# Kernel optimization log

Measured on AMD Instinct MI355X. Metric: run time of the kernel, lower is better.

## Reference

```python
import jax, jax.numpy as jnp
import numpy as np

B, S, D, H = 4, 1024, 1024, 16
DK = D // H
N_REL = 5


def setup_inputs() -> dict:
    key = jax.random.key(0)
    ks = jax.random.split(key, 16)
    p = lambda k, shape: (jax.random.normal(k, shape, dtype=jnp.float32) * 0.02)
    return {
        "x": jax.random.normal(ks[0], (B, S, D), dtype=jnp.float32),
        "relation_matrix": jax.random.randint(ks[1], (S, S), 0, N_REL, dtype=jnp.int32),
        "mask": jax.random.randint(ks[2], (B, 1, S, S), 0, 2, dtype=jnp.int32),
        "Wq": p(ks[3], (D, D)), "bq": p(ks[4], (D,)),
        "Wk": p(ks[5], (D, D)), "bk": p(ks[6], (D,)),
        "Wv": p(ks[7], (D, D)), "bv": p(ks[8], (D,)),
        "Wo": p(ks[9], (D, D)), "bo": p(ks[10], (D,)),
        "rel_table": p(ks[11], (N_REL, DK)),
        "gamma": jnp.ones((D,), dtype=jnp.float32),
        "beta": jnp.zeros((D,), dtype=jnp.float32),
    }


def reference(x, relation_matrix, mask, Wq, bq, Wk, bk, Wv, bv, Wo, bo, rel_table, gamma, beta):
    b, s = x.shape[0], x.shape[1]
    residual = x
    # projections -> [B, H, S, DK]
    def proj(W, bias):
        return (x @ W + bias).reshape(b, s, H, DK).transpose(0, 2, 1, 3)
    Q, K, V = proj(Wq, bq), proj(Wk, bk), proj(Wv, bv)
    scores = jnp.einsum('bhid,bhjd->bhij', Q, K) / jnp.sqrt(jnp.float32(DK))
    # relation-embedding additive bias: gather [S,S,DK] then contract with Q
    rel_emb = rel_table[relation_matrix]               # [S, S, DK]
    rel_scores = jnp.einsum('bhid,ijd->bhij', Q, rel_emb)
    scores = scores + rel_scores * 0.5
    scores = jnp.where(mask == 0, jnp.float32(-1e9), scores)
    attention = jax.nn.softmax(scores, axis=-1)
    context = jnp.einsum('bhij,bhjd->bhid', attention, V)
    context = context.transpose(0, 2, 1, 3).reshape(b, s, D)
    output = context @ Wo + bo
    # layer norm (eps = 1e-5, torch default)
    y = output + residual
    mu = jnp.mean(y, axis=-1, keepdims=True)
    var = jnp.mean(jnp.square(y - mu), axis=-1, keepdims=True)
    return (y - mu) * jax.lax.rsqrt(var + 1e-5) * gamma + beta
```

## Files before the change

### kernel.cpp

```cpp
#include <hip/hip_runtime.h>
#include <hip/hip_bf16.h>

typedef unsigned short u16;
typedef unsigned int u32;
typedef unsigned char u8;
typedef __attribute__((ext_vector_type(8))) short short8;
typedef __attribute__((ext_vector_type(4))) float f32x4;

__device__ __forceinline__ float b2f(u16 u) {
    union { float f; u32 i; } z; z.i = ((u32)u) << 16; return z.f;
}
__device__ __forceinline__ u16 f2b(float f) {
    union { float f; u32 i; } z; z.f = f;
    u32 i = z.i;
    u32 r = (i + 0x7FFFu + ((i >> 16) & 1u)) >> 16;
    return (u16)r;
}
__device__ __forceinline__ float ldf(const void* p, size_t i, int f) {
    return f ? ((const float*)p)[i] : b2f(((const u16*)p)[i]);
}
__device__ __forceinline__ void gload_lds16(const void* g, void* l) {
    __builtin_amdgcn_global_load_lds(
        (const __attribute__((address_space(1))) u32*)g,
        (__attribute__((address_space(3))) u32*)l,
        16, 0, 0);
}

struct P14 { const void* p[14]; };
struct S14 { int s[14]; };

__global__ __launch_bounds__(256) void classify_stats(P14 ptrs, S14 szs, int* stats)
{
    __shared__ int   wsm[4], wzr[4], wag[4], way[4], wjk[4];
    __shared__ float wme[4], wmo[4];
    int i = blockIdx.x;
    int t = threadIdx.x, lane = t & 63, w = t >> 6;
    const u16* p16 = (const u16*)ptrs.p[i];
    const u32* p32 = (const u32*)ptrs.p[i];
    int n = szs.s[i];
    int n16 = n < 4096 ? n : 4096;
    int n32 = n16 >> 1;
    int small = 1, zero = 1, allg = 1, anyg = 0, junk = 0;
    float maxe = 0.f, maxo = 0.f;
    for (int k = t; k < n32; k += 256) if (p32[k] >= 8u) small = 0;
    for (int k = t; k < n16; k += 256) {
        u16 ww = p16[k];
        if (ww != 0) zero = 0;
        if (ww == 0x3F80u) anyg = 1;
        else if (ww != 0) allg = 0;
        float a = fabsf(b2f(ww));
        if (k & 1) { if (a < 1e30f && a > maxo) maxo = a; }
        else { if (!(a < 100.0f)) junk++; else if (a > maxe) maxe = a; }
    }
#pragma unroll
    for (int s = 1; s < 64; s <<= 1) {
        small &= __shfl_xor(small, s);
        zero  &= __shfl_xor(zero, s);
        allg  &= __shfl_xor(allg, s);
        anyg  |= __shfl_xor(anyg, s);
        junk  += __shfl_xor(junk, s);
        maxe   = fmaxf(maxe, __shfl_xor(maxe, s));
        maxo   = fmaxf(maxo, __shfl_xor(maxo, s));
    }
    if (lane == 0) { wsm[w]=small; wzr[w]=zero; wag[w]=allg; way[w]=anyg; wjk[w]=junk; wme[w]=maxe; wmo[w]=maxo; }
    __syncthreads();
    if (t == 0) {
        int sm=1,zr=1,ag=1,ay=0,jk=0; float me=0.f,mo=0.f;
        for (int q=0;q<4;++q){ sm&=wsm[q]; zr&=wzr[q]; ag&=wag[q]; ay|=way[q]; jk+=wjk[q]; me=fmaxf(me,wme[q]); mo=fmaxf(mo,wmo[q]); }
        stats[i*8+0]=sm; stats[i*8+1]=zr; stats[i*8+2]=(ag&&ay)?1:0; stats[i*8+3]=jk;
        stats[i*8+4]=__float_as_int(me); stats[i*8+5]=__float_as_int(mo);
    }
}

__global__ __launch_bounds__(64) void classify_bind(S14 szs, const int* stats, int* cls)
{
    if (threadIdx.x != 0) return;
    int xi = -1, mi = -1, ri = -1, rt = -1, gi = -1, bi = -1;
    int wv[4] = {-1,-1,-1,-1}; int nw = 0;
    int bs[4] = {-1,-1,-1,-1}; int nb = 0;
    for (int i = 0; i < 14; ++i) {
        int s = szs.s[i];
        int sm = stats[i*8+0], zr = stats[i*8+1];
        if (s == 4194304) { if (sm) mi = i; else xi = i; }
        else if (s == 1048576) { if (sm) ri = i; else if (nw < 4) wv[nw++] = i; }
        else if (s == 320) rt = i;
        else if (s == 1024) {
            if (zr) bi = i;
            else if (stats[i*8+2]) gi = i;
            else if (nb < 4) bs[nb++] = i;
        }
    }
    bool ok = (xi >= 0) && (mi >= 0) && (ri >= 0) && (rt >= 0) && (gi >= 0) && (bi >= 0)
           && (nw == 4) && (nb == 4);
    if (ok) {
        cls[0] = xi; cls[1] = ri; cls[2] = mi;
        cls[3] = wv[0]; cls[5] = wv[1]; cls[7] = wv[2]; cls[9] = wv[3];
        cls[4] = bs[0]; cls[6] = bs[1]; cls[8] = bs[2]; cls[10] = bs[3];
        cls[11] = rt; cls[12] = gi; cls[13] = bi;
    } else {
        for (int r = 0; r < 14; ++r) cls[r] = r;
    }
    const int froles[12] = {0,3,4,5,6,7,8,9,10,11,12,13};
    for (int r = 0; r < 12; ++r) {
        int role = froles[r]; int idx = cls[role];
        float me = __int_as_float(stats[idx*8+4]);
        float mo = __int_as_float(stats[idx*8+5]);
        cls[16 + role] = (stats[idx*8+3] > 0) || (me == 0.f && mo > 0.f);
    }
    cls[30] = ok ? 1 : 0;
}

__global__ __launch_bounds__(256) void cvt_x_flex(P14 ptrs, const int* cls, u16* xb) {
    const void* x = ptrs.p[cls[0]];
    int f = cls[16];
    int idx = (blockIdx.x * 256 + threadIdx.x) << 2;
    union { u16 u[4]; uint2 v2; } o;
    if (f) {
        float4 v = *(const float4*)((const float*)x + idx);
        o.u[0] = f2b(v.x); o.u[1] = f2b(v.y); o.u[2] = f2b(v.z); o.u[3] = f2b(v.w);
    } else {
        o.v2 = *(const uint2*)((const u16*)x + idx);
    }
    *(uint2*)&xb[idx] = o.v2;
}

__global__ __launch_bounds__(256) void transposeW_flex(P14 ptrs, const int* cls,
                                                       u16* WT3, u16* WoT)
{
    int z = blockIdx.z;
    const void* W = ptrs.p[cls[3 + 2 * z]];
    int f = cls[16 + 3 + 2 * z];
    u16* WT = (z < 3) ? (WT3 + ((size_t)z << 20)) : WoT;
    __shared__ u16 tile[64][72];
    int t = threadIdx.x;
    int n0 = blockIdx.x << 6, k0 = blockIdx.y << 6;
    int r = t >> 2, c = (t & 3) << 4;
    size_t base = (size_t)(k0 + r) * 1024 + n0 + c;
    if (f) {
        const float* src = (const float*)W + base;
#pragma unroll
        for (int x = 0; x < 16; ++x) tile[r][c + x] = f2b(src[x]);
    } else {
        const u16* src = (const u16*)W + base;
#pragma unroll
        for (int x = 0; x < 16; ++x) tile[r][c + x] = src[x];
    }
    __syncthreads();
    union { u16 u[16]; uint4 v[2]; } tmp;
#pragma unroll
    for (int x = 0; x < 16; ++x) tmp.u[x] = tile[c + x][r];
    *(uint4*)&WT[(size_t)(n0 + r) * 1024 + k0 + c]     = tmp.v[0];
    *(uint4*)&WT[(size_t)(n0 + r) * 1024 + k0 + c + 8] = tmp.v[1];
}

__global__ __launch_bounds__(256) void transposeV(const u16* __restrict__ Vb,
                                                  u16* __restrict__ VT)
{
    __shared__ u16 tile[64][72];
    int bh = blockIdx.y, j0 = blockIdx.x << 6;
    const u16* src = Vb + ((size_t)bh << 16);
    u16* dst = VT + ((size_t)bh << 16);
    int t = threadIdx.x, r = t >> 2, c = (t & 3) << 4;
    const u16* s = src + (size_t)(j0 + r) * 64 + c;
    *(uint4*)&tile[r][c]     = *(const uint4*)s;
    *(uint4*)&tile[r][c + 8] = *(const uint4*)(s + 8);
    __syncthreads();
    union { u16 u[16]; uint4 v[2]; } tmp;
#pragma unroll
    for (int x = 0; x < 16; ++x) tmp.u[x] = tile[c + x][r];
    int swz = (r & 7) << 3;
    int c2 = c ^ (swz & 48);
    int hsw = (swz >> 3) & 1;
    u16* d = dst + (size_t)r * 1024 + j0 + c2;
    *(uint4*)d       = tmp.v[hsw];
    *(uint4*)(d + 8) = tmp.v[1 - hsw];
}

__global__ __launch_bounds__(256) void qrel_k(
    const u16* __restrict__ Q, P14 ptrs, const int* cls, float* __restrict__ Qrel)
{
    __shared__ float rt[5][64];
    const void* rel_table = ptrs.p[cls[11]];
    int f9 = cls[16 + 11];
    int t = threadIdx.x;
    for (int p = t; p < 320; p += 256) ((float*)rt)[p] = ldf(rel_table, p, f9);
    __syncthreads();
    int row = blockIdx.x * 256 + t;
    const u16* qrow = Q + ((size_t)row << 6);
    float a0=0.f, a1=0.f, a2=0.f, a3=0.f, a4=0.f;
#pragma unroll
    for (int k8 = 0; k8 < 64; k8 += 8) {
        union { uint4 v; u16 u[8]; } qq;
        qq.v = *(const uint4*)(qrow + k8);
#pragma unroll
        for (int e = 0; e < 8; ++e) {
            float qv = b2f(qq.u[e]);
            a0 += qv * rt[0][k8 + e];
            a1 += qv * rt[1][k8 + e];
            a2 += qv * rt[2][k8 + e];
            a3 += qv * rt[3][k8 + e];
            a4 += qv * rt[4][k8 + e];
        }
    }
    const float S = 0.5f * 1.44269504f;
    float4 o0 = {a0 * S, a1 * S, a2 * S, a3 * S};
    float4 o1 = {a4 * S, -1e9f, -1e9f, -1e9f};
    *(float4*)&Qrel[(size_t)row * 8]     = o0;
    *(float4*)&Qrel[(size_t)row * 8 + 4] = o1;
}

__global__ __launch_bounds__(256) void gemm128_qkv(
    const u16* __restrict__ X, const u16* __restrict__ WT3,
    P14 ptrs, const int* cls,
    u16* __restrict__ Qb, u16* __restrict__ Kb, u16* __restrict__ Vb)
{
    int z = blockIdx.z;
    const u16* WT = WT3 + ((size_t)z << 20);
    const void* biasp = ptrs.p[cls[4 + 2 * z]];
    int fb = cls[16 + 4 + 2 * z];
    u16* outp = (z == 0) ? Qb : (z == 1) ? Kb : Vb;
    int n0 = blockIdx.x << 7, m0 = blockIdx.y << 7;
    __shared__ u16 As[2][128][4][8];
    __shared__ u16 Bs[2][128][4][8];
    int t = threadIdx.x, lane = t & 63, w = t >> 6;
    int m = lane & 15, quad = lane >> 4;
    int wm = (w >> 1) << 6, wn = (w & 1) << 6;
    int r1 = t >> 2, r2 = 64 + r1, k4 = t & 3;
    const u16* xa  = &X [(size_t)(m0 + r1) * 1024 + k4 * 8];
    const u16* xa2 = &X [(size_t)(m0 + r2) * 1024 + k4 * 8];
    const u16* wb  = &WT[(size_t)(n0 + r1) * 1024 + k4 * 8];
    const u16* wb2 = &WT[(size_t)(n0 + r2) * 1024 + k4 * 8];
    f32x4 acc[4][4];
#pragma unroll
    for (int i = 0; i < 4; ++i)
#pragma unroll
        for (int j = 0; j < 4; ++j) acc[i][j] = (f32x4){0.f,0.f,0.f,0.f};

    auto stage = [&](int buf, int k0) {
        gload_lds16(xa  + k0, &As[buf][r1][k4][0]);
        gload_lds16(xa2 + k0, &As[buf][r2][k4][0]);
        gload_lds16(wb  + k0, &Bs[buf][r1][k4][0]);
        gload_lds16(wb2 + k0, &Bs[buf][r2][k4][0]);
    };
    stage(0, 0);
    __syncthreads();
    int cur = 0;
    for (int k0 = 0; k0 < 1024; k0 += 32) {
        if (k0 + 32 < 1024) stage(cur ^ 1, k0 + 32);
        short8 af[4], bf[4];
#pragma unroll
        for (int mb = 0; mb < 4; ++mb) af[mb] = *(const short8*)&As[cur][wm + mb*16 + m][quad][0];
#pragma unroll
        for (int nb = 0; nb < 4; ++nb) bf[nb] = *(const short8*)&Bs[cur][wn + nb*16 + m][quad][0];
#pragma unroll
        for (int mb = 0; mb < 4; ++mb)
#pragma unroll
            for (int nb = 0; nb < 4; ++nb)
                acc[mb][nb] = __builtin_amdgcn_mfma_f32_16x16x32_bf16(af[mb], bf[nb], acc[mb][nb], 0, 0, 0);
        __syncthreads();
        cur ^= 1;
    }
#pragma unroll
    for (int nb = 0; nb < 4; ++nb) {
        int gn = n0 + wn + nb*16 + m;
        int h = gn >> 6, dk = gn & 63;
        float bb = ldf(biasp, gn, fb);
#pragma unroll
        for (int mb = 0; mb < 4; ++mb)
#pragma unroll
            for (int r = 0; r < 4; ++r) {
                int gm = m0 + wm + mb*16 + (quad << 2) + r;
                int b = gm >> 10, s = gm & 1023;
                int dk2 = (z == 1) ? (dk ^ (((quad * 4 + r) & 7) << 3)) : dk;
                outp[((size_t)((b * 16 + h) << 10) + s) * 64 + dk2] = f2b(acc[mb][nb][r] + bb);
            }
    }
}

__global__ __launch_bounds__(256) void gemm128_out(
    const u16* __restrict__ A, const u16* __restrict__ WT,
    P14 ptrs, const int* cls, float* __restrict__ y)
{
    const void* bo   = ptrs.p[cls[10]];
    const void* Xres = ptrs.p[cls[0]];
    int f8 = cls[16 + 10], f0 = cls[16];
    int n0 = blockIdx.x << 7, m0 = blockIdx.y << 7;
    __shared__ u16 As[2][128][4][8];
    __shared__ u16 Bs[2][128][4][8];
    int t = threadIdx.x, lane = t & 63, w = t >> 6;
    int m = lane & 15, quad = lane >> 4;
    int wm = (w >> 1) << 6, wn = (w & 1) << 6;
    int r1 = t >> 2, r2 = 64 + r1, k4 = t & 3;
    const u16* xa  = &A [(size_t)(m0 + r1) * 1024 + k4 * 8];
    const u16* xa2 = &A [(size_t)(m0 + r2) * 1024 + k4 * 8];
    const u16* wb  = &WT[(size_t)(n0 + r1) * 1024 + k4 * 8];
    const u16* wb2 = &WT[(size_t)(n0 + r2) * 1024 + k4 * 8];
    f32x4 acc[4][4];
#pragma unroll
    for (int i = 0; i < 4; ++i)
#pragma unroll
        for (int j = 0; j < 4; ++j) acc[i][j] = (f32x4){0.f,0.f,0.f,0.f};

    auto stage = [&](int buf, int k0) {
        gload_lds16(xa  + k0, &As[buf][r1][k4][0]);
        gload_lds16(xa2 + k0, &As[buf][r2][k4][0]);
        gload_lds16(wb  + k0, &Bs[buf][r1][k4][0]);
        gload_lds16(wb2 + k0, &Bs[buf][r2][k4][0]);
    };
    stage(0, 0);
    __syncthreads();
    int cur = 0;
    for (int k0 = 0; k0 < 1024; k0 += 32) {
        if (k0 + 32 < 1024) stage(cur ^ 1, k0 + 32);
        short8 af[4], bf[4];
#pragma unroll
        for (int mb = 0; mb < 4; ++mb) af[mb] = *(const short8*)&As[cur][wm + mb*16 + m][quad][0];
#pragma unroll
        for (int nb = 0; nb < 4; ++nb) bf[nb] = *(const short8*)&Bs[cur][wn + nb*16 + m][quad][0];
#pragma unroll
        for (int mb = 0; mb < 4; ++mb)
#pragma unroll
            for (int nb = 0; nb < 4; ++nb)
                acc[mb][nb] = __builtin_amdgcn_mfma_f32_16x16x32_bf16(af[mb], bf[nb], acc[mb][nb], 0, 0, 0);
        __syncthreads();
        cur ^= 1;
    }
#pragma unroll
    for (int nb = 0; nb < 4; ++nb) {
        int gn = n0 + wn + nb*16 + m;
        float bb = ldf(bo, gn, f8);
#pragma unroll
        for (int mb = 0; mb < 4; ++mb)
#pragma unroll
            for (int r = 0; r < 4; ++r) {
                int gm = m0 + wm + mb*16 + (quad << 2) + r;
                size_t idx = (size_t)gm * 1024 + gn;
                y[idx] = acc[mb][nb][r] + bb + ldf(Xres, idx, f0);
            }
    }
}

__global__ __launch_bounds__(256) void make_codes(P14 ptrs, const int* cls, u8* codes)
{
    const int* relmat = (const int*)ptrs.p[cls[1]];
    const int* maskp  = (const int*)ptrs.p[cls[2]];
    int bid = blockIdx.x;
    int b = bid >> 8, ti = (bid >> 4) & 15, tj = bid & 15;
    int t = threadIdx.x, lane = t & 63, w = t >> 6;
    int m = lane & 15, quad = lane >> 4;
    const int* mb = maskp + ((size_t)b << 20);
    union { uint4 v; u8 c[16]; } out;
#pragma unroll
    for (int jb = 0; jb < 4; ++jb) {
        int j = tj * 64 + jb * 16 + m;
#pragma unroll
        for (int r = 0; r < 4; ++r) {
            int i = ti * 64 + w * 16 + (quad << 2) + r;
            size_t off = (size_t)i * 1024 + j;
            out.c[jb * 4 + r] = mb[off] ? (u8)relmat[off] : (u8)5;
        }
    }
    ((uint4*)codes)[(size_t)bid * 256 + t] = out.v;
}

__global__ __launch_bounds__(256) void attn_mfma(
    const u16* __restrict__ Q, const u16* __restrict__ K, const u16* __restrict__ VT,
    const float* __restrict__ Qrel, const u8* __restrict__ codes, u16* __restrict__ ctx)
{
    int raw = blockIdx.x;
    int bid = (raw & 7) * 128 + (raw >> 3);
    int bh = bid >> 4, ti = bid & 15;
    int i0 = ti << 6;
    int b = bh >> 4, h = bh & 15;
    const u16* Qp = Q  + ((size_t)bh << 16);
    const u16* Kp = K  + ((size_t)bh << 16);
    const u16* Vp = VT + ((size_t)bh << 16);
    const uint4* ctile = (const uint4*)codes + ((size_t)((b * 16 + ti) * 16) << 8);

    __shared__ u16 Ks[2][64][64];
    __shared__ u16 Vt[2][64][64];
    __shared__ u16 Pls[64][72];
    __shared__ float Qrl[64][9];

    int t = threadIdx.x, lane = t & 63, w = t >> 6;
    int m = lane & 15, quad = lane >> 4;

    {
        float2 qv = *(const float2*)&Qrel[(((size_t)bh << 10) + i0) * 8 + (t << 1)];
        Qrl[t >> 2][(t & 3) << 1]       = qv.x;
        Qrl[t >> 2][((t & 3) << 1) + 1] = qv.y;
    }

    short8 qfrag0, qfrag1;
    {
        const u16* qr = Qp + (size_t)(i0 + w * 16 + m) * 64 + quad * 8;
        qfrag0 = *(const short8*)qr;
        qfrag1 = *(const short8*)(qr + 32);
    }
    f32x4 O[4];
    float l_part[4];
#pragma unroll
    for (int d = 0; d < 4; ++d) O[d] = (f32x4){0.f,0.f,0.f,0.f};
#pragma unroll
    for (int r = 0; r < 4; ++r) l_part[r] = 0.f;

    int srow = t >> 3, scol8 = (t & 7) << 3;
    const u16* ks0 = Kp + (size_t)srow * 64 + scol8;
    const u16* ks1 = ks0 + 32 * 64;
    const u16* vs0 = Vp + (size_t)srow * 1024 + scol8;
    const u16* vs1 = vs0 + 32 * 1024;

    auto stage = [&](int buf, int j0) {
        gload_lds16(ks0 + (size_t)j0 * 64, &Ks[buf][srow][scol8]);
        gload_lds16(ks1 + (size_t)j0 * 64, &Ks[buf][srow + 32][scol8]);
        gload_lds16(vs0 + j0, &Vt[buf][srow][scol8]);
        gload_lds16(vs1 + j0, &Vt[buf][srow + 32][scol8]);
    };

    const float SC = 0.125f * 1.44269504f;
    int kx = (m & 7) << 3;

    stage(0, 0);
    uint4 cN = ctile[t];
    __syncthreads();
    int cur = 0;

    for (int j0 = 0; j0 < 1024; j0 += 64) {
        if (j0 + 64 < 1024) stage(cur ^ 1, j0 + 64);
        union { uint4 v; u8 c[16]; } cd;
        cd.v = cN;
        if (j0 + 64 < 1024) cN = ctile[(((j0 + 64) >> 6) << 8) + t];

        f32x4 acc[4];
#pragma unroll
        for (int jb = 0; jb < 4; ++jb) {
            acc[jb] = (f32x4){0.f,0.f,0.f,0.f};
            short8 kb0 = *(const short8*)&Ks[cur][jb * 16 + m][(quad * 8) ^ kx];
            short8 kb1 = *(const short8*)&Ks[cur][jb * 16 + m][(32 + quad * 8) ^ kx];
            acc[jb] = __builtin_amdgcn_mfma_f32_16x16x32_bf16(qfrag0, kb0, acc[jb], 0, 0, 0);
            acc[jb] = __builtin_amdgcn_mfma_f32_16x16x32_bf16(qfrag1, kb1, acc[jb], 0, 0, 0);
        }
        float sc[4][4];
#pragma unroll
        for (int jb = 0; jb < 4; ++jb) {
#pragma unroll
            for (int r = 0; r < 4; ++r) {
                int il = w * 16 + (quad << 2) + r;
                float p = exp2f(acc[jb][r] * SC + Qrl[il][cd.c[jb * 4 + r]]);
                sc[jb][r] = p;
                l_part[r] += p;
            }
        }
#pragma unroll
        for (int jb = 0; jb < 4; ++jb)
#pragma unroll
            for (int r = 0; r < 4; ++r)
                Pls[w * 16 + (quad << 2) + r][jb * 16 + m] = f2b(sc[jb][r]);
        short8 pa0 = *(const short8*)&Pls[w * 16 + m][quad * 8];
        short8 pa1 = *(const short8*)&Pls[w * 16 + m][quad * 8 + 32];
#pragma unroll
        for (int db = 0; db < 4; ++db) {
            short8 vb0 = *(const short8*)&Vt[cur][db * 16 + m][(quad * 8) ^ kx];
            short8 vb1 = *(const short8*)&Vt[cur][db * 16 + m][(32 + quad * 8) ^ kx];
            O[db] = __builtin_amdgcn_mfma_f32_16x16x32_bf16(pa0, vb0, O[db], 0, 0, 0);
            O[db] = __builtin_amdgcn_mfma_f32_16x16x32_bf16(pa1, vb1, O[db], 0, 0, 0);
        }
        __syncthreads();
        cur ^= 1;
    }
    float linv[4];
#pragma unroll
    for (int r = 0; r < 4; ++r) {
        float l = l_part[r];
        l += __shfl_xor(l, 1);
        l += __shfl_xor(l, 2);
        l += __shfl_xor(l, 4);
        l += __shfl_xor(l, 8);
        linv[r] = 1.0f / fmaxf(l, 1e-35f);
    }
#pragma unroll
    for (int db = 0; db < 4; ++db)
#pragma unroll
        for (int r = 0; r < 4; ++r) {
            int il = w * 16 + (quad << 2) + r;
            size_t addr = ((size_t)(b * 1024 + i0 + il)) * 1024 + h * 64 + db * 16 + m;
            ctx[addr] = f2b(O[db][r] * linv[r]);
        }
}

__global__ __launch_bounds__(256) void ln_k(
    float* __restrict__ y, P14 ptrs, const int* cls)
{
    const void* gamma = ptrs.p[cls[12]];
    const void* beta  = ptrs.p[cls[13]];
    int f10 = cls[16 + 12], f11 = cls[16 + 13];
    int row = blockIdx.x, t = threadIdx.x;
    float4 v = *(const float4*)&y[(size_t)row * 1024 + (t << 2)];
    float s = v.x + v.y + v.z + v.w;
#pragma unroll
    for (int mm = 1; mm < 64; mm <<= 1) s += __shfl_xor(s, mm);
    __shared__ float sm[8];
    int w = t >> 6, lane = t & 63;
    if (lane == 0) sm[w] = s;
    __syncthreads();
    float mu = (sm[0] + sm[1] + sm[2] + sm[3]) * (1.0f / 1024.0f);
    float dx = v.x - mu, dy = v.y - mu, dz = v.z - mu, dw = v.w - mu;
    float q = dx * dx + dy * dy + dz * dz + dw * dw;
#pragma unroll
    for (int mm = 1; mm < 64; mm <<= 1) q += __shfl_xor(q, mm);
    if (lane == 0) sm[4 + w] = q;
    __syncthreads();
    float var = (sm[4] + sm[5] + sm[6] + sm[7]) * (1.0f / 1024.0f);
    float rs = rsqrtf(var + 1e-5f);
    int c = t << 2;
    float4 o;
    o.x = dx * rs * ldf(gamma, c,     f10) + ldf(beta, c,     f11);
    o.y = dy * rs * ldf(gamma, c + 1, f10) + ldf(beta, c + 1, f11);
    o.z = dz * rs * ldf(gamma, c + 2, f10) + ldf(beta, c + 2, f11);
    o.w = dw * rs * ldf(gamma, c + 3, f10) + ldf(beta, c + 3, f11);
    *(float4*)&y[(size_t)row * 1024 + c] = o;
}

extern "C" void kernel_launch(void* const* d_in, const int* in_sizes, int n_in,
                              void* d_out, int out_size, void* d_ws, size_t ws_size,
                              hipStream_t stream) {
    (void)out_size; (void)ws_size;
    P14 ptrs; S14 szs;
    for (int i = 0; i < 14; ++i) {
        ptrs.p[i] = (i < n_in) ? d_in[i] : d_in[0];
        szs.s[i]  = (i < n_in) ? in_sizes[i] : 0;
    }
    float* out = (float*)d_out;

    char* ws = (char*)d_ws;
    const size_t MB = 1u << 20;
    u16*   WT3   = (u16*)(ws);
    u16*   WoT   = (u16*)(ws + 6 * MB);
    u16*   Xb    = (u16*)(ws + 8 * MB);
    u16*   VbT   = (u16*)(ws + 8 * MB);
    u16*   Qb    = (u16*)(ws + 16 * MB);
    u16*   Kb    = (u16*)(ws + 24 * MB);
    u16*   Vb    = (u16*)(ws + 32 * MB);
    u16*   ctx   = (u16*)(ws + 32 * MB);
    u8*    codes = (u8*)(ws);
    float* Qrel  = (float*)(ws + 4 * MB);
    int*   cls   = (int*)(ws + 40 * MB);
    int*   stats = (int*)(ws + 40 * MB + 512);

    classify_stats<<<14, 256, 0, stream>>>(ptrs, szs, stats);
    classify_bind<<<1, 64, 0, stream>>>(szs, stats, cls);
    cvt_x_flex<<<4096, 256, 0, stream>>>(ptrs, cls, Xb);
    transposeW_flex<<<dim3(16, 16, 4), 256, 0, stream>>>(ptrs, cls, WT3, WoT);
    gemm128_qkv<<<dim3(8, 32, 3), 256, 0, stream>>>(Xb, WT3, ptrs, cls, Qb, Kb, Vb);
    transposeV<<<dim3(16, 64), 256, 0, stream>>>(Vb, VbT);
    qrel_k<<<256, 256, 0, stream>>>(Qb, ptrs, cls, Qrel);
    make_codes<<<1024, 256, 0, stream>>>(ptrs, cls, codes);
    attn_mfma<<<1024, 256, 0, stream>>>(Qb, Kb, VbT, Qrel, codes, ctx);
    gemm128_out<<<dim3(8, 32), 256, 0, stream>>>(ctx, WoT, ptrs, cls, out);
    ln_k<<<4096, 256, 0, stream>>>(out, ptrs, cls);
}
```

Baseline: 301.2 us.

## Fuse V transpose into QKV GEMM epilogue, remap block order, shrink out-GEMM tiles

The QKV GEMM now writes V straight into the transposed, swizzled layout the attention kernel reads, so the separate transposeV launch and its round trip through memory go away. The QKV and output GEMM grids become 1D with a remapped block order, and the output GEMM moves to 64x128 tiles with twice as many blocks to fill more CUs. In attention, V loses its LDS double buffer: the next V tile is loaded after the PV MFMAs, with an extra barrier, to cut LDS use. The single-buffered V adds a barrier and exposes V load latency, and the transposed epilogue writes are less coalesced.

```diff
diff --git a/kernel.cpp b/kernel.cpp
--- a/kernel.cpp
+++ b/kernel.cpp
@@ -153,29 +153,6 @@
     *(uint4*)&WT[(size_t)(n0 + r) * 1024 + k0 + c + 8] = tmp.v[1];
 }
 
-__global__ __launch_bounds__(256) void transposeV(const u16* __restrict__ Vb,
-                                                  u16* __restrict__ VT)
-{
-    __shared__ u16 tile[64][72];
-    int bh = blockIdx.y, j0 = blockIdx.x << 6;
-    const u16* src = Vb + ((size_t)bh << 16);
-    u16* dst = VT + ((size_t)bh << 16);
-    int t = threadIdx.x, r = t >> 2, c = (t & 3) << 4;
-    const u16* s = src + (size_t)(j0 + r) * 64 + c;
-    *(uint4*)&tile[r][c]     = *(const uint4*)s;
-    *(uint4*)&tile[r][c + 8] = *(const uint4*)(s + 8);
-    __syncthreads();
-    union { u16 u[16]; uint4 v[2]; } tmp;
-#pragma unroll
-    for (int x = 0; x < 16; ++x) tmp.u[x] = tile[c + x][r];
-    int swz = (r & 7) << 3;
-    int c2 = c ^ (swz & 48);
-    int hsw = (swz >> 3) & 1;
-    u16* d = dst + (size_t)r * 1024 + j0 + c2;
-    *(uint4*)d       = tmp.v[hsw];
-    *(uint4*)(d + 8) = tmp.v[1 - hsw];
-}
-
 __global__ __launch_bounds__(256) void qrel_k(
     const u16* __restrict__ Q, P14 ptrs, const int* cls, float* __restrict__ Qrel)
 {
@@ -212,14 +189,14 @@
 __global__ __launch_bounds__(256) void gemm128_qkv(
     const u16* __restrict__ X, const u16* __restrict__ WT3,
     P14 ptrs, const int* cls,
-    u16* __restrict__ Qb, u16* __restrict__ Kb, u16* __restrict__ Vb)
-{
-    int z = blockIdx.z;
+    u16* __restrict__ Qb, u16* __restrict__ Kb, u16* __restrict__ VTb)
+{
+    int o = (blockIdx.x & 7) * 96 + (blockIdx.x >> 3);
+    int z = (o >> 3) % 3;
+    int n0 = (o & 7) << 7, m0 = (o / 24) << 7;
     const u16* WT = WT3 + ((size_t)z << 20);
     const void* biasp = ptrs.p[cls[4 + 2 * z]];
     int fb = cls[16 + 4 + 2 * z];
-    u16* outp = (z == 0) ? Qb : (z == 1) ? Kb : Vb;
-    int n0 = blockIdx.x << 7, m0 = blockIdx.y << 7;
     __shared__ u16 As[2][128][4][8];
     __shared__ u16 Bs[2][128][4][8];
     int t = threadIdx.x, lane = t & 63, w = t >> 6;
@@ -260,50 +237,70 @@
         __syncthreads();
         cur ^= 1;
     }
-#pragma unroll
-    for (int nb = 0; nb < 4; ++nb) {
-        int gn = n0 + wn + nb*16 + m;
-        int h = gn >> 6, dk = gn & 63;
-        float bb = ldf(biasp, gn, fb);
-#pragma unroll
-        for (int mb = 0; mb < 4; ++mb)
-#pragma unroll
-            for (int r = 0; r < 4; ++r) {
-                int gm = m0 + wm + mb*16 + (quad << 2) + r;
-                int b = gm >> 10, s = gm & 1023;
-                int dk2 = (z == 1) ? (dk ^ (((quad * 4 + r) & 7) << 3)) : dk;
-                outp[((size_t)((b * 16 + h) << 10) + s) * 64 + dk2] = f2b(acc[mb][nb][r] + bb);
+    if (z == 2) {
+#pragma unroll
+        for (int nb = 0; nb < 4; ++nb) {
+            int gn = n0 + wn + nb*16 + m;
+            int h = gn >> 6, dk = gn & 63;
+            float bv = ldf(biasp, gn, fb);
+            int sx = (dk & 7) << 3;
+#pragma unroll
+            for (int mb = 0; mb < 4; ++mb) {
+                int gmBase = m0 + wm + mb*16 + (quad << 2);
+                int bI = gmBase >> 10, sB = gmBase & 1023;
+                int pos = (sB & ~63) | ((sB & 63) ^ sx);
+                union { u16 u[4]; uint2 v; } o4;
+#pragma unroll
+                for (int r = 0; r < 4; ++r) o4.u[r] = f2b(acc[mb][nb][r] + bv);
+                *(uint2*)&VTb[((size_t)(bI * 16 + h) << 16) + dk * 1024 + pos] = o4.v;
             }
-    }
-}
-
-__global__ __launch_bounds__(256) void gemm128_out(
+        }
+    } else {
+        u16* outp = (z == 0) ? Qb : Kb;
+#pragma unroll
+        for (int nb = 0; nb < 4; ++nb) {
+            int gn = n0 + wn + nb*16 + m;
+            int h = gn >> 6, dk = gn & 63;
+            float bv = ldf(biasp, gn, fb);
+#pragma unroll
+            for (int mb = 0; mb < 4; ++mb)
+#pragma unroll
+                for (int r = 0; r < 4; ++r) {
+                    int gm = m0 + wm + mb*16 + (quad << 2) + r;
+                    int bI = gm >> 10, s = gm & 1023;
+                    int dk2 = (z == 1) ? (dk ^ (((quad * 4 + r) & 7) << 3)) : dk;
+                    outp[((size_t)((bI * 16 + h) << 10) + s) * 64 + dk2] = f2b(acc[mb][nb][r] + bv);
+                }
+        }
+    }
+}
+
+__global__ __launch_bounds__(256) void gemm_out64(
     const u16* __restrict__ A, const u16* __restrict__ WT,
     P14 ptrs, const int* cls, float* __restrict__ y)
 {
     const void* bo   = ptrs.p[cls[10]];
     const void* Xres = ptrs.p[cls[0]];
     int f8 = cls[16 + 10], f0 = cls[16];
-    int n0 = blockIdx.x << 7, m0 = blockIdx.y << 7;
-    __shared__ u16 As[2][128][4][8];
+    int o = (blockIdx.x & 7) * 64 + (blockIdx.x >> 3);
+    int n0 = (o & 7) << 7, m0 = (o >> 3) << 6;
+    __shared__ u16 As[2][64][4][8];
     __shared__ u16 Bs[2][128][4][8];
     int t = threadIdx.x, lane = t & 63, w = t >> 6;
     int m = lane & 15, quad = lane >> 4;
-    int wm = (w >> 1) << 6, wn = (w & 1) << 6;
+    int wm = (w >> 1) << 5, wn = (w & 1) << 6;
     int r1 = t >> 2, r2 = 64 + r1, k4 = t & 3;
     const u16* xa  = &A [(size_t)(m0 + r1) * 1024 + k4 * 8];
-    const u16* xa2 = &A [(size_t)(m0 + r2) * 1024 + k4 * 8];
     const u16* wb  = &WT[(size_t)(n0 + r1) * 1024 + k4 * 8];
     const u16* wb2 = &WT[(size_t)(n0 + r2) * 1024 + k4 * 8];
-    f32x4 acc[4][4];
-#pragma unroll
-    for (int i = 0; i < 4; ++i)
+    f32x4 acc[2][4];
+#pragma unroll
+    for (int i = 0; i < 2; ++i)
 #pragma unroll
         for (int j = 0; j < 4; ++j) acc[i][j] = (f32x4){0.f,0.f,0.f,0.f};
 
     auto stage = [&](int buf, int k0) {
         gload_lds16(xa  + k0, &As[buf][r1][k4][0]);
-        gload_lds16(xa2 + k0, &As[buf][r2][k4][0]);
         gload_lds16(wb  + k0, &Bs[buf][r1][k4][0]);
         gload_lds16(wb2 + k0, &Bs[buf][r2][k4][0]);
     };
@@ -312,13 +309,13 @@
     int cur = 0;
     for (int k0 = 0; k0 < 1024; k0 += 32) {
         if (k0 + 32 < 1024) stage(cur ^ 1, k0 + 32);
-        short8 af[4], bf[4];
-#pragma unroll
-        for (int mb = 0; mb < 4; ++mb) af[mb] = *(const short8*)&As[cur][wm + mb*16 + m][quad][0];
+        short8 af[2], bf[4];
+#pragma unroll
+        for (int mb = 0; mb < 2; ++mb) af[mb] = *(const short8*)&As[cur][wm + mb*16 + m][quad][0];
 #pragma unroll
         for (int nb = 0; nb < 4; ++nb) bf[nb] = *(const short8*)&Bs[cur][wn + nb*16 + m][quad][0];
 #pragma unroll
-        for (int mb = 0; mb < 4; ++mb)
+        for (int mb = 0; mb < 2; ++mb)
 #pragma unroll
             for (int nb = 0; nb < 4; ++nb)
                 acc[mb][nb] = __builtin_amdgcn_mfma_f32_16x16x32_bf16(af[mb], bf[nb], acc[mb][nb], 0, 0, 0);
@@ -330,7 +327,7 @@
         int gn = n0 + wn + nb*16 + m;
         float bb = ldf(bo, gn, f8);
 #pragma unroll
-        for (int mb = 0; mb < 4; ++mb)
+        for (int mb = 0; mb < 2; ++mb)
 #pragma unroll
             for (int r = 0; r < 4; ++r) {
                 int gm = m0 + wm + mb*16 + (quad << 2) + r;
@@ -378,7 +375,7 @@
     const uint4* ctile = (const uint4*)codes + ((size_t)((b * 16 + ti) * 16) << 8);
 
     __shared__ u16 Ks[2][64][64];
-    __shared__ u16 Vt[2][64][64];
+    __shared__ u16 Vt[64][64];
     __shared__ u16 Pls[64][72];
     __shared__ float Qrl[64][9];
 
@@ -410,26 +407,27 @@
     const u16* vs0 = Vp + (size_t)srow * 1024 + scol8;
     const u16* vs1 = vs0 + 32 * 1024;
 
-    auto stage = [&](int buf, int j0) {
+    auto stageK = [&](int buf, int j0) {
         gload_lds16(ks0 + (size_t)j0 * 64, &Ks[buf][srow][scol8]);
         gload_lds16(ks1 + (size_t)j0 * 64, &Ks[buf][srow + 32][scol8]);
-        gload_lds16(vs0 + j0, &Vt[buf][srow][scol8]);
-        gload_lds16(vs1 + j0, &Vt[buf][srow + 32][scol8]);
+    };
+    auto stageV = [&](int j0) {
+        gload_lds16(vs0 + j0, &Vt[srow][scol8]);
+        gload_lds16(vs1 + j0, &Vt[srow + 32][scol8]);
     };
 
     const float SC = 0.125f * 1.44269504f;
     int kx = (m & 7) << 3;
 
-    stage(0, 0);
+    stageK(0, 0);
+    stageV(0);
     uint4 cN = ctile[t];
     __syncthreads();
     int cur = 0;
 
     for (int j0 = 0; j0 < 1024; j0 += 64) {
-        if (j0 + 64 < 1024) stage(cur ^ 1, j0 + 64);
-        union { uint4 v; u8 c[16]; } cd;
-        cd.v = cN;
-        if (j0 + 64 < 1024) cN = ctile[(((j0 + 64) >> 6) << 8) + t];
+        bool next = (j0 + 64 < 1024);
+        if (next) stageK(cur ^ 1, j0 + 64);
 
         f32x4 acc[4];
 #pragma unroll
@@ -440,6 +438,10 @@
             acc[jb] = __builtin_amdgcn_mfma_f32_16x16x32_bf16(qfrag0, kb0, acc[jb], 0, 0, 0);
             acc[jb] = __builtin_amdgcn_mfma_f32_16x16x32_bf16(qfrag1, kb1, acc[jb], 0, 0, 0);
         }
+        union { uint4 v; u8 c[16]; } cd;
+        cd.v = cN;
+        if (next) cN = ctile[(((j0 + 64) >> 6) << 8) + t];
+
         float sc[4][4];
 #pragma unroll
         for (int jb = 0; jb < 4; ++jb) {
@@ -456,16 +458,21 @@
 #pragma unroll
             for (int r = 0; r < 4; ++r)
                 Pls[w * 16 + (quad << 2) + r][jb * 16 + m] = f2b(sc[jb][r]);
+
+        __syncthreads();
+
         short8 pa0 = *(const short8*)&Pls[w * 16 + m][quad * 8];
         short8 pa1 = *(const short8*)&Pls[w * 16 + m][quad * 8 + 32];
 #pragma unroll
         for (int db = 0; db < 4; ++db) {
-            short8 vb0 = *(const short8*)&Vt[cur][db * 16 + m][(quad * 8) ^ kx];
-            short8 vb1 = *(const short8*)&Vt[cur][db * 16 + m][(32 + quad * 8) ^ kx];
+            short8 vb0 = *(const short8*)&Vt[db * 16 + m][(quad * 8) ^ kx];
+            short8 vb1 = *(const short8*)&Vt[db * 16 + m][(32 + quad * 8) ^ kx];
             O[db] = __builtin_amdgcn_mfma_f32_16x16x32_bf16(pa0, vb0, O[db], 0, 0, 0);
             O[db] = __builtin_amdgcn_mfma_f32_16x16x32_bf16(pa1, vb1, O[db], 0, 0, 0);
         }
+
         __syncthreads();
+        if (next) stageV(j0 + 64);
         cur ^= 1;
     }
     float linv[4];
@@ -537,11 +544,10 @@
     u16*   WT3   = (u16*)(ws);
     u16*   WoT   = (u16*)(ws + 6 * MB);
     u16*   Xb    = (u16*)(ws + 8 * MB);
-    u16*   VbT   = (u16*)(ws + 8 * MB);
     u16*   Qb    = (u16*)(ws + 16 * MB);
     u16*   Kb    = (u16*)(ws + 24 * MB);
-    u16*   Vb    = (u16*)(ws + 32 * MB);
-    u16*   ctx   = (u16*)(ws + 32 * MB);
+    u16*   VTb   = (u16*)(ws + 32 * MB);
+    u16*   ctx   = (u16*)(ws + 8 * MB);
     u8*    codes = (u8*)(ws);
     float* Qrel  = (float*)(ws + 4 * MB);
     int*   cls   = (int*)(ws + 40 * MB);
@@ -551,11 +557,10 @@
     classify_bind<<<1, 64, 0, stream>>>(szs, stats, cls);
     cvt_x_flex<<<4096, 256, 0, stream>>>(ptrs, cls, Xb);
     transposeW_flex<<<dim3(16, 16, 4), 256, 0, stream>>>(ptrs, cls, WT3, WoT);
-    gemm128_qkv<<<dim3(8, 32, 3), 256, 0, stream>>>(Xb, WT3, ptrs, cls, Qb, Kb, Vb);
-    transposeV<<<dim3(16, 64), 256, 0, stream>>>(Vb, VbT);
+    gemm128_qkv<<<768, 256, 0, stream>>>(Xb, WT3, ptrs, cls, Qb, Kb, VTb);
     qrel_k<<<256, 256, 0, stream>>>(Qb, ptrs, cls, Qrel);
     make_codes<<<1024, 256, 0, stream>>>(ptrs, cls, codes);
-    attn_mfma<<<1024, 256, 0, stream>>>(Qb, Kb, VbT, Qrel, codes, ctx);
-    gemm128_out<<<dim3(8, 32), 256, 0, stream>>>(ctx, WoT, ptrs, cls, out);
+    attn_mfma<<<1024, 256, 0, stream>>>(Qb, Kb, VTb, Qrel, codes, ctx);
+    gemm_out64<<<512, 256, 0, stream>>>(ctx, WoT, ptrs, cls, out);
     ln_k<<<4096, 256, 0, stream>>>(out, ptrs, cls);
 }
```

Result: faster. 289.8 us (-3.8%).
